# Kernel tuning notes

Measured on AMD Instinct MI355X. Metric: run time of the kernel, lower is better.

Reference implementation:

```python
import jax, jax.numpy as jnp
import numpy as np

B, N, D_IN, D_OUT = 8, 2048, 256, 128
ROW_ZERO = 85 - 10  # hardcoded in original: a[:, 0:85-10] = 0 (zeros rows, dim 1)
NEG_BIG = -9.0e15
EPS = 1e-12  # F.normalize eps


def setup_inputs() -> dict:
    key = jax.random.key(0)
    k1, k2, k3, k4 = jax.random.split(key, 4)
    h = jax.random.normal(k1, (B, N, D_IN), dtype=jnp.float32)
    adj = jax.random.randint(k2, (B, N, N), 0, 2, dtype=jnp.int32)
    adj_eye = jax.random.randint(k3, (B, N, N), 0, 2, dtype=jnp.int32)
    # xavier_uniform with gain=1.414 for W [in, out]
    limit = 1.414 * np.sqrt(6.0 / (D_IN + D_OUT))
    W = jax.random.uniform(k4, (D_IN, D_OUT), minval=-limit, maxval=limit, dtype=jnp.float32)
    return {"h": h, "adj": adj, "adj_eye": adj_eye, "W": W}


def reference(h, adj, adj_eye, W):
    # Wh: [B, N, D_OUT]
    Wh = jnp.matmul(h, W)
    # L2-normalize along feature dim (F.normalize semantics: x / max(||x||, eps))
    norm = jnp.maximum(jnp.linalg.norm(Wh, axis=-1, keepdims=True), EPS)
    Whn = Wh / norm
    # dense cosine-similarity scores: [B, N, N]
    score = jnp.einsum("bnd,bmd->bnm", Whn, Whn)
    # double-sort top-k emulation (faithful to original, incl. row-wise zeroing bug)
    a_sorted = jnp.sort(score, axis=-1)
    idx1 = jnp.argsort(score, axis=-1)
    a_sorted = a_sorted.at[:, 0:ROW_ZERO, :].set(0.0)
    idx2 = jnp.argsort(idx1, axis=-1)  # inverse permutation
    attscore = jnp.take_along_axis(a_sorted, idx2, axis=-1)
    # adjacency mask + softmax over neighbors
    e = jnp.where(adj_eye > 0, attscore, NEG_BIG)
    attention = jax.nn.softmax(e, axis=-1)
    # (dropout is identity in eval mode)
    h_prime = jnp.matmul(attention, Wh)
    return jax.nn.elu(h_prime)
```

## Files before the change

### kernel.cpp

```cpp
#include <hip/hip_runtime.h>
#include <stdint.h>

#define NN   2048
#define DD   128
#define DIN  256
#define ROWZ 75

typedef float f32x4 __attribute__((ext_vector_type(4)));
typedef short bf16x8 __attribute__((ext_vector_type(8)));
typedef unsigned int u32x2 __attribute__((ext_vector_type(2)));

__device__ __forceinline__ unsigned short f2bf(float x){
  union { float f; unsigned int u; } v; v.f = x;
  unsigned int u = v.u;
  u += 0x7fffu + ((u >> 16) & 1u);
  return (unsigned short)(u >> 16);
}
__device__ __forceinline__ float bf2f(unsigned short b){
  union { float f; unsigned int u; } v; v.u = ((unsigned int)b) << 16;
  return v.f;
}

__launch_bounds__(256, 2)
__global__ void wh_kernel(const float* __restrict__ h, const float* __restrict__ W,
                          unsigned short* __restrict__ whn, unsigned short* __restrict__ whT)
{
  __shared__ float hs[32][36];
  __shared__ float Ws[32][128];
  __shared__ float ssp[32][33];
  __shared__ float sinv[32];

  const int t  = threadIdx.x;
  const int bid = blockIdx.x;
  const int r0 = ((bid & 7) << 11) | ((bid >> 3) << 5);
  const int r4 = (t >> 5) * 4;
  const int d4 = (t & 31) * 4;

  float acc[4][4];
#pragma unroll
  for (int i = 0; i < 4; ++i)
#pragma unroll
    for (int j = 0; j < 4; ++j) acc[i][j] = 0.f;

  const int lrow = t >> 3;
  const int lkb  = (t & 7) * 4;
  const int wk   = t >> 3;
  const int wd   = (t & 7) * 16;

  f32x4 ph = *(const f32x4*)(h + (size_t)(r0 + lrow) * DIN + lkb);
  f32x4 pW[4];
  {
    const float* ws = W + (size_t)wk * DD + wd;
#pragma unroll
    for (int e = 0; e < 4; ++e) pW[e] = ((const f32x4*)ws)[e];
  }

  for (int kt = 0; kt < 8; ++kt){
    __syncthreads();
#pragma unroll
    for (int e = 0; e < 4; ++e) hs[lkb + e][lrow] = ph[e];
    {
      f32x4* dst = (f32x4*)&Ws[wk][wd];
#pragma unroll
      for (int e = 0; e < 4; ++e) dst[e] = pW[e];
    }
    __syncthreads();

    if (kt < 7){
      ph = *(const f32x4*)(h + (size_t)(r0 + lrow) * DIN + (kt+1)*32 + lkb);
      const float* ws = W + (size_t)((kt+1)*32 + wk) * DD + wd;
#pragma unroll
      for (int e = 0; e < 4; ++e) pW[e] = ((const f32x4*)ws)[e];
    }

#pragma unroll
    for (int k = 0; k < 32; ++k){
      f32x4 w4 = *(const f32x4*)&Ws[k][d4];
      f32x4 ha = *(const f32x4*)&hs[k][r4];
#pragma unroll
      for (int i = 0; i < 4; ++i)
#pragma unroll
        for (int j = 0; j < 4; ++j)
          acc[i][j] += ha[i] * w4[j];
    }
  }

#pragma unroll
  for (int i = 0; i < 4; ++i){
    float s = acc[i][0]*acc[i][0] + acc[i][1]*acc[i][1]
            + acc[i][2]*acc[i][2] + acc[i][3]*acc[i][3];
    ssp[r4 + i][t & 31] = s;
  }
  __syncthreads();
  if (t < 32){
    float ss = 0.f;
#pragma unroll
    for (int c = 0; c < 32; ++c) ss += ssp[t][c];
    sinv[t] = 1.0f / fmaxf(sqrtf(ss), 1e-12f);
  }
  __syncthreads();

  const int bb = r0 >> 11;
  const int n0 = (r0 & 2047) + r4;

#pragma unroll
  for (int i = 0; i < 4; ++i){
    const float inv = sinv[r4 + i];
    unsigned int lo = (unsigned int)f2bf(acc[i][0]*inv) | ((unsigned int)f2bf(acc[i][1]*inv) << 16);
    unsigned int hi = (unsigned int)f2bf(acc[i][2]*inv) | ((unsigned int)f2bf(acc[i][3]*inv) << 16);
    u32x2 pk = { lo, hi };
    *(u32x2*)(whn + (size_t)(r0 + r4 + i) * DD + d4) = pk;
  }
#pragma unroll
  for (int j = 0; j < 4; ++j){
    u32x2 pk;
#pragma unroll
    for (int e = 0; e < 2; ++e)
      pk[e] = (unsigned int)f2bf(acc[2*e][j]) | ((unsigned int)f2bf(acc[2*e + 1][j]) << 16);
    *(u32x2*)(whT + ((size_t)(bb * DD + d4 + j)) * NN + n0) = pk;
  }
}

__launch_bounds__(512, 2)
__global__ void attn_kernel(const unsigned short* __restrict__ whn,
                            const unsigned short* __restrict__ whT,
                            const int* __restrict__ adje,
                            float* __restrict__ out)
{
  __shared__ unsigned short Kt[2][128 * 128];
  __shared__ unsigned short Vt[2][128 * 128];
  __shared__ unsigned short Pbuf[8][32 * 40];
  __shared__ float linv_s[64];

  const int t    = threadIdx.x;
  const int w    = t >> 6;
  const int l    = t & 63;
  const int quad = l >> 4;
  const int l16  = l & 15;
  const int qh   = w >> 2;
  const int ms   = w & 3;
  const int b     = blockIdx.x & 7;
  const int qbase = (blockIdx.x >> 3) * 64;

  const unsigned short* whn_b = whn + (size_t)b * NN * DD;
  const unsigned short* whT_b = whT + (size_t)b * DD * NN;
  const int*            adj_b = adje + (size_t)b * NN * NN;

#define STAGE(M0, CC)                                                          \
  if (w < 4){                                                                  \
    _Pragma("unroll")                                                          \
    for (int ii = 0; ii < 8; ++ii){                                            \
      const int row = w*32 + ii*4 + (l >> 4);                                  \
      const unsigned short* src = whn_b + (size_t)((M0) + row) * DD            \
                                  + (l16 ^ (row & 7)) * 8;                     \
      __builtin_amdgcn_global_load_lds(                                        \
          (const __attribute__((address_space(1))) void*)src,                  \
          (__attribute__((address_space(3))) void*)&Kt[CC][(w*32 + ii*4)*128], \
          16, 0, 0);                                                           \
    }                                                                          \
  } else {                                                                     \
    _Pragma("unroll")                                                          \
    for (int ii = 0; ii < 8; ++ii){                                            \
      const int dv = (w-4)*32 + ii*4 + (l >> 4);                               \
      const unsigned short* src = whT_b + (size_t)dv * NN + (M0)               \
                                  + (l16 ^ (dv & 7)) * 8;                      \
      __builtin_amdgcn_global_load_lds(                                        \
          (const __attribute__((address_space(1))) void*)src,                  \
          (__attribute__((address_space(3))) void*)&Vt[CC][((w-4)*32+ii*4)*128],\
          16, 0, 0);                                                           \
    }                                                                          \
  }

  bf16x8 qf[2][4];
#pragma unroll
  for (int s = 0; s < 2; ++s)
#pragma unroll
    for (int kc = 0; kc < 4; ++kc)
      qf[s][kc] = *(const bf16x8*)(whn_b + (size_t)(qbase + qh*32 + s*16 + l16) * DD + kc*32 + quad*8);

  f32x4 oacc[2][8];
  float lacc[2][4];
#pragma unroll
  for (int s = 0; s < 2; ++s){
#pragma unroll
    for (int dt = 0; dt < 8; ++dt) oacc[s][dt] = (f32x4){0.f, 0.f, 0.f, 0.f};
#pragma unroll
    for (int r = 0; r < 4; ++r) lacc[s][r] = 0.f;
  }

  unsigned short* const Pw = &Pbuf[w][0];

  int av[2][2][4];
#pragma unroll
  for (int f = 0; f < 2; ++f)
#pragma unroll
    for (int s = 0; s < 2; ++s)
#pragma unroll
      for (int r = 0; r < 4; ++r)
        av[f][s][r] = adj_b[(size_t)(qbase + qh*32 + s*16 + quad*4 + r) * NN + ms*32 + f*16 + l16];
  STAGE(0, 0)
  __syncthreads();

  for (int it = 0; it < 16; ++it){
    const int m0  = it * 128;
    const int cur = it & 1;

    int avn[2][2][4];
    if (it < 15){
      const int mn = m0 + 128;
#pragma unroll
      for (int f = 0; f < 2; ++f)
#pragma unroll
        for (int s = 0; s < 2; ++s)
#pragma unroll
          for (int r = 0; r < 4; ++r)
            avn[f][s][r] = adj_b[(size_t)(qbase + qh*32 + s*16 + quad*4 + r) * NN + mn + ms*32 + f*16 + l16];
      STAGE(mn, cur ^ 1)
    }

    bf16x8 kf[2][4];
#pragma unroll
    for (int f = 0; f < 2; ++f)
#pragma unroll
      for (int kc = 0; kc < 4; ++kc){
        const int row = ms*32 + f*16 + l16;
        kf[f][kc] = *(const bf16x8*)&Kt[cur][row*128 + (((kc*4 + quad) ^ (l16 & 7)) * 8)];
      }
#pragma unroll
    for (int f = 0; f < 2; ++f){
#pragma unroll
      for (int s = 0; s < 2; ++s){
        f32x4 sc = (f32x4){0.f, 0.f, 0.f, 0.f};
#pragma unroll
        for (int kc = 0; kc < 4; ++kc)
          sc = __builtin_amdgcn_mfma_f32_16x16x32_bf16(qf[s][kc], kf[f][kc], sc, 0, 0, 0);
#pragma unroll
        for (int r = 0; r < 4; ++r){
          const int qrow = qbase + qh*32 + s*16 + quad*4 + r;
          float sv = (qrow < ROWZ) ? 0.f : sc[r];
          float p32 = (av[f][s][r] > 0) ? __expf(sv) : 0.f;
          unsigned short pb = f2bf(p32);
          lacc[s][r] += bf2f(pb);
          Pw[(s*16 + quad*4 + r) * 40 + f*16 + l16] = pb;
        }
      }
    }

    bf16x8 pfr0 = *(const bf16x8*)&Pw[(l16) * 40 + quad*8];
    bf16x8 pfr1 = *(const bf16x8*)&Pw[(16 + l16) * 40 + quad*8];
    __builtin_amdgcn_s_setprio(1);
#pragma unroll
    for (int dt = 0; dt < 8; ++dt){
      const int d = dt*16 + l16;
      bf16x8 vf = *(const bf16x8*)&Vt[cur][d*128 + (((ms*4 + quad) ^ (l16 & 7)) * 8)];
      oacc[0][dt] = __builtin_amdgcn_mfma_f32_16x16x32_bf16(pfr0, vf, oacc[0][dt], 0, 0, 0);
      oacc[1][dt] = __builtin_amdgcn_mfma_f32_16x16x32_bf16(pfr1, vf, oacc[1][dt], 0, 0, 0);
    }
    __builtin_amdgcn_s_setprio(0);

    __builtin_amdgcn_sched_barrier(0);
    asm volatile("s_waitcnt vmcnt(0)" ::: "memory");
    __builtin_amdgcn_sched_barrier(0);
    __builtin_amdgcn_s_barrier();
    __builtin_amdgcn_sched_barrier(0);

    if (it < 15){
#pragma unroll
      for (int f = 0; f < 2; ++f)
#pragma unroll
        for (int s = 0; s < 2; ++s)
#pragma unroll
          for (int r = 0; r < 4; ++r)
            av[f][s][r] = avn[f][s][r];
    }
  }

  {
    float* fl = (float*)&Pbuf[0][0];
#pragma unroll
    for (int s = 0; s < 2; ++s)
#pragma unroll
      for (int r = 0; r < 4; ++r)
        fl[(qh*32 + s*16 + quad*4 + r) * 64 + ms*16 + l16] = lacc[s][r];
  }
  __syncthreads();
  if (t < 64){
    const float* fl = (const float*)&Pbuf[0][0];
    float sum = 0.f;
#pragma unroll
    for (int c = 0; c < 64; ++c) sum += fl[t * 64 + c];
    linv_s[t] = 1.0f / sum;
  }

  float* const owf = (float*)&Kt[0][0];
  for (int s = 0; s < 2; ++s){
    __syncthreads();
#pragma unroll
    for (int dt = 0; dt < 8; ++dt)
#pragma unroll
      for (int r = 0; r < 4; ++r)
        owf[w*2048 + (quad*4 + r)*128 + dt*16 + l16] = oacc[s][dt][r];
    __syncthreads();
#pragma unroll
    for (int j = 0; j < 8; ++j){
      const int o     = j*512 + t;
      const int row32 = o >> 7;
      const int d     = o & 127;
      const int qh2   = row32 >> 4;
      const int r16   = row32 & 15;
      float v = owf[(qh2*4 + 0)*2048 + r16*128 + d]
              + owf[(qh2*4 + 1)*2048 + r16*128 + d]
              + owf[(qh2*4 + 2)*2048 + r16*128 + d]
              + owf[(qh2*4 + 3)*2048 + r16*128 + d];
      const int qrl = qh2*32 + s*16 + r16;
      v *= linv_s[qrl];
      v = (v > 0.f) ? v : expm1f(v);
      out[(size_t)(b*NN + qbase + qrl) * DD + d] = v;
    }
  }
#undef STAGE
}

extern "C" void kernel_launch(void* const* d_in, const int* in_sizes, int n_in,
                              void* d_out, int out_size, void* d_ws, size_t ws_size,
                              hipStream_t stream)
{
  const float* h       = (const float*)d_in[0];
  const int*   adj_eye = (const int*)d_in[2];
  const float* W       = (const float*)d_in[3];
  float*       out     = (float*)d_out;

  unsigned short* whn  = (unsigned short*)d_ws;
  unsigned short* whT  = whn + (size_t)16384 * 128;

  wh_kernel<<<512, 256, 0, stream>>>(h, W, whn, whT);
  attn_kernel<<<256, 512, 0, stream>>>(whn, whT, adj_eye, out);
}
```

Measured before the change: 285.8 us.

## Load K and V fragments directly from global, drop LDS double-buffering and barriers

Removes the double-buffered LDS staging of K and V tiles and the per-iteration vmcnt wait and block barrier. Each wave now loads its K and V MFMA fragments straight from global memory, relying on L2/L1 for reuse. Adjacency values are read as int2 pairs with a permuted column mapping, and the P row sum now accumulates the fp32 values instead of the bf16-rounded ones. This cuts LDS use and barrier stalls, but it increases redundant global/L2 traffic across waves and exposes load latency with no explicit prefetch.

Result: slower. 319.0 us (+11.6%).

```diff
diff --git a/kernel.cpp b/kernel.cpp
--- a/kernel.cpp
+++ b/kernel.cpp
@@ -8,6 +8,7 @@
 
 typedef float f32x4 __attribute__((ext_vector_type(4)));
 typedef short bf16x8 __attribute__((ext_vector_type(8)));
+typedef int   i32x2  __attribute__((ext_vector_type(2)));
 typedef unsigned int u32x2 __attribute__((ext_vector_type(2)));
 
 __device__ __forceinline__ unsigned short f2bf(float x){
@@ -15,10 +16,6 @@
   unsigned int u = v.u;
   u += 0x7fffu + ((u >> 16) & 1u);
   return (unsigned short)(u >> 16);
-}
-__device__ __forceinline__ float bf2f(unsigned short b){
-  union { float f; unsigned int u; } v; v.u = ((unsigned int)b) << 16;
-  return v.f;
 }
 
 __launch_bounds__(256, 2)
@@ -127,9 +124,7 @@
                             const int* __restrict__ adje,
                             float* __restrict__ out)
 {
-  __shared__ unsigned short Kt[2][128 * 128];
-  __shared__ unsigned short Vt[2][128 * 128];
-  __shared__ unsigned short Pbuf[8][32 * 40];
+  __shared__ float smem[16384];
   __shared__ float linv_s[64];
 
   const int t    = threadIdx.x;
@@ -146,30 +141,7 @@
   const unsigned short* whT_b = whT + (size_t)b * DD * NN;
   const int*            adj_b = adje + (size_t)b * NN * NN;
 
-#define STAGE(M0, CC)                                                          \
-  if (w < 4){                                                                  \
-    _Pragma("unroll")                                                          \
-    for (int ii = 0; ii < 8; ++ii){                                            \
-      const int row = w*32 + ii*4 + (l >> 4);                                  \
-      const unsigned short* src = whn_b + (size_t)((M0) + row) * DD            \
-                                  + (l16 ^ (row & 7)) * 8;                     \
-      __builtin_amdgcn_global_load_lds(                                        \
-          (const __attribute__((address_space(1))) void*)src,                  \
-          (__attribute__((address_space(3))) void*)&Kt[CC][(w*32 + ii*4)*128], \
-          16, 0, 0);                                                           \
-    }                                                                          \
-  } else {                                                                     \
-    _Pragma("unroll")                                                          \
-    for (int ii = 0; ii < 8; ++ii){                                            \
-      const int dv = (w-4)*32 + ii*4 + (l >> 4);                               \
-      const unsigned short* src = whT_b + (size_t)dv * NN + (M0)               \
-                                  + (l16 ^ (dv & 7)) * 8;                      \
-      __builtin_amdgcn_global_load_lds(                                        \
-          (const __attribute__((address_space(1))) void*)src,                  \
-          (__attribute__((address_space(3))) void*)&Vt[CC][((w-4)*32+ii*4)*128],\
-          16, 0, 0);                                                           \
-    }                                                                          \
-  }
+  unsigned short* const Pw = (unsigned short*)smem + w * (32 * 40);
 
   bf16x8 qf[2][4];
 #pragma unroll
@@ -188,95 +160,86 @@
     for (int r = 0; r < 4; ++r) lacc[s][r] = 0.f;
   }
 
-  unsigned short* const Pw = &Pbuf[w][0];
-
-  int av[2][2][4];
-#pragma unroll
-  for (int f = 0; f < 2; ++f)
-#pragma unroll
-    for (int s = 0; s < 2; ++s)
-#pragma unroll
-      for (int r = 0; r < 4; ++r)
-        av[f][s][r] = adj_b[(size_t)(qbase + qh*32 + s*16 + quad*4 + r) * NN + ms*32 + f*16 + l16];
-  STAGE(0, 0)
-  __syncthreads();
+  bool zr[2][4];
+#pragma unroll
+  for (int s = 0; s < 2; ++s)
+#pragma unroll
+    for (int r = 0; r < 4; ++r)
+      zr[s][r] = (qbase + qh*32 + s*16 + quad*4 + r) < ROWZ;
+
+  i32x2 av[2][4];
+#pragma unroll
+  for (int s = 0; s < 2; ++s)
+#pragma unroll
+    for (int r = 0; r < 4; ++r)
+      av[s][r] = *(const i32x2*)(adj_b + (size_t)(qbase + qh*32 + s*16 + quad*4 + r) * NN + ms*32 + 2*l16);
 
   for (int it = 0; it < 16; ++it){
-    const int m0  = it * 128;
-    const int cur = it & 1;
-
-    int avn[2][2][4];
+    const int m0 = it * 128;
+
+    bf16x8 kf[2][4];
+#pragma unroll
+    for (int f = 0; f < 2; ++f)
+#pragma unroll
+      for (int kc = 0; kc < 4; ++kc)
+        kf[f][kc] = *(const bf16x8*)(whn_b + (size_t)(m0 + ms*32 + 2*l16 + f) * DD + kc*32 + quad*8);
+
+    i32x2 avn[2][4];
     if (it < 15){
       const int mn = m0 + 128;
 #pragma unroll
-      for (int f = 0; f < 2; ++f)
-#pragma unroll
-        for (int s = 0; s < 2; ++s)
-#pragma unroll
-          for (int r = 0; r < 4; ++r)
-            avn[f][s][r] = adj_b[(size_t)(qbase + qh*32 + s*16 + quad*4 + r) * NN + mn + ms*32 + f*16 + l16];
-      STAGE(mn, cur ^ 1)
-    }
-
-    bf16x8 kf[2][4];
-#pragma unroll
-    for (int f = 0; f < 2; ++f)
+      for (int s = 0; s < 2; ++s)
+#pragma unroll
+        for (int r = 0; r < 4; ++r)
+          avn[s][r] = *(const i32x2*)(adj_b + (size_t)(qbase + qh*32 + s*16 + quad*4 + r) * NN + mn + ms*32 + 2*l16);
+    }
+
+#pragma unroll
+    for (int s = 0; s < 2; ++s){
+      f32x4 sc0 = (f32x4){0.f,0.f,0.f,0.f};
+      f32x4 sc1 = (f32x4){0.f,0.f,0.f,0.f};
 #pragma unroll
       for (int kc = 0; kc < 4; ++kc){
-        const int row = ms*32 + f*16 + l16;
-        kf[f][kc] = *(const bf16x8*)&Kt[cur][row*128 + (((kc*4 + quad) ^ (l16 & 7)) * 8)];
+        sc0 = __builtin_amdgcn_mfma_f32_16x16x32_bf16(qf[s][kc], kf[0][kc], sc0, 0, 0, 0);
+        sc1 = __builtin_amdgcn_mfma_f32_16x16x32_bf16(qf[s][kc], kf[1][kc], sc1, 0, 0, 0);
       }
 #pragma unroll
-    for (int f = 0; f < 2; ++f){
-#pragma unroll
-      for (int s = 0; s < 2; ++s){
-        f32x4 sc = (f32x4){0.f, 0.f, 0.f, 0.f};
-#pragma unroll
-        for (int kc = 0; kc < 4; ++kc)
-          sc = __builtin_amdgcn_mfma_f32_16x16x32_bf16(qf[s][kc], kf[f][kc], sc, 0, 0, 0);
-#pragma unroll
-        for (int r = 0; r < 4; ++r){
-          const int qrow = qbase + qh*32 + s*16 + quad*4 + r;
-          float sv = (qrow < ROWZ) ? 0.f : sc[r];
-          float p32 = (av[f][s][r] > 0) ? __expf(sv) : 0.f;
-          unsigned short pb = f2bf(p32);
-          lacc[s][r] += bf2f(pb);
-          Pw[(s*16 + quad*4 + r) * 40 + f*16 + l16] = pb;
-        }
+      for (int r = 0; r < 4; ++r){
+        float sv0 = zr[s][r] ? 0.f : sc0[r];
+        float sv1 = zr[s][r] ? 0.f : sc1[r];
+        float p0 = (av[s][r].x > 0) ? __expf(sv0) : 0.f;
+        float p1 = (av[s][r].y > 0) ? __expf(sv1) : 0.f;
+        lacc[s][r] += p0 + p1;
+        unsigned int pk = (unsigned int)f2bf(p0) | ((unsigned int)f2bf(p1) << 16);
+        *(unsigned int*)&Pw[(s*16 + quad*4 + r) * 40 + 2*l16] = pk;
       }
     }
 
     bf16x8 pfr0 = *(const bf16x8*)&Pw[(l16) * 40 + quad*8];
     bf16x8 pfr1 = *(const bf16x8*)&Pw[(16 + l16) * 40 + quad*8];
+    bf16x8 vf[8];
+#pragma unroll
+    for (int dt = 0; dt < 8; ++dt)
+      vf[dt] = *(const bf16x8*)(whT_b + (size_t)(dt*16 + l16) * NN + m0 + ms*32 + quad*8);
     __builtin_amdgcn_s_setprio(1);
 #pragma unroll
     for (int dt = 0; dt < 8; ++dt){
-      const int d = dt*16 + l16;
-      bf16x8 vf = *(const bf16x8*)&Vt[cur][d*128 + (((ms*4 + quad) ^ (l16 & 7)) * 8)];
-      oacc[0][dt] = __builtin_amdgcn_mfma_f32_16x16x32_bf16(pfr0, vf, oacc[0][dt], 0, 0, 0);
-      oacc[1][dt] = __builtin_amdgcn_mfma_f32_16x16x32_bf16(pfr1, vf, oacc[1][dt], 0, 0, 0);
+      oacc[0][dt] = __builtin_amdgcn_mfma_f32_16x16x32_bf16(pfr0, vf[dt], oacc[0][dt], 0, 0, 0);
+      oacc[1][dt] = __builtin_amdgcn_mfma_f32_16x16x32_bf16(pfr1, vf[dt], oacc[1][dt], 0, 0, 0);
     }
     __builtin_amdgcn_s_setprio(0);
 
-    __builtin_amdgcn_sched_barrier(0);
-    asm volatile("s_waitcnt vmcnt(0)" ::: "memory");
-    __builtin_amdgcn_sched_barrier(0);
-    __builtin_amdgcn_s_barrier();
-    __builtin_amdgcn_sched_barrier(0);
-
-    if (it < 15){
-#pragma unroll
-      for (int f = 0; f < 2; ++f)
-#pragma unroll
-        for (int s = 0; s < 2; ++s)
-#pragma unroll
-          for (int r = 0; r < 4; ++r)
-            av[f][s][r] = avn[f][s][r];
-    }
-  }
+#pragma unroll
+    for (int s = 0; s < 2; ++s)
+#pragma unroll
+      for (int r = 0; r < 4; ++r)
+        av[s][r] = avn[s][r];
+  }
+
+  __syncthreads();
 
   {
-    float* fl = (float*)&Pbuf[0][0];
+    float* fl = smem;
 #pragma unroll
     for (int s = 0; s < 2; ++s)
 #pragma unroll
@@ -285,14 +248,14 @@
   }
   __syncthreads();
   if (t < 64){
-    const float* fl = (const float*)&Pbuf[0][0];
+    const float* fl = smem;
     float sum = 0.f;
 #pragma unroll
     for (int c = 0; c < 64; ++c) sum += fl[t * 64 + c];
     linv_s[t] = 1.0f / sum;
   }
 
-  float* const owf = (float*)&Kt[0][0];
+  float* const owf = smem;
   for (int s = 0; s < 2; ++s){
     __syncthreads();
 #pragma unroll
@@ -318,7 +281,6 @@
       out[(size_t)(b*NN + qbase + qrl) * DD + d] = v;
     }
   }
-#undef STAGE
 }
 
 extern "C" void kernel_launch(void* const* d_in, const int* in_sizes, int n_in,
```

## Compute Wh projection with split-bf16 MFMA instead of scalar FP32 FMA

Applied to the files above, without the earlier changes.

The h·W projection kernel now splits each fp32 operand into bf16 hi and lo parts and accumulates three bf16 MFMA products, giving near-fp32 accuracy on the matrix cores instead of scalar FMAs. It computes both Wh and its transpose directly in MFMA layouts and reduces the row norms with shuffles. Blocks change to 64 rows and 512 threads. The projection is a small share of total time and the output stores are narrower and less coalesced, so the overall gain is bounded.

After: 282.7 us. No clear change (-1.1%).

```diff
diff --git a/kernel.cpp b/kernel.cpp
--- a/kernel.cpp
+++ b/kernel.cpp
@@ -21,104 +21,122 @@
   return v.f;
 }
 
-__launch_bounds__(256, 2)
+__launch_bounds__(512, 2)
 __global__ void wh_kernel(const float* __restrict__ h, const float* __restrict__ W,
                           unsigned short* __restrict__ whn, unsigned short* __restrict__ whT)
 {
-  __shared__ float hs[32][36];
-  __shared__ float Ws[32][128];
-  __shared__ float ssp[32][33];
-  __shared__ float sinv[32];
-
-  const int t  = threadIdx.x;
-  const int bid = blockIdx.x;
-  const int r0 = ((bid & 7) << 11) | ((bid >> 3) << 5);
-  const int r4 = (t >> 5) * 4;
-  const int d4 = (t & 31) * 4;
-
-  float acc[4][4];
-#pragma unroll
-  for (int i = 0; i < 4; ++i)
-#pragma unroll
-    for (int j = 0; j < 4; ++j) acc[i][j] = 0.f;
-
-  const int lrow = t >> 3;
-  const int lkb  = (t & 7) * 4;
-  const int wk   = t >> 3;
-  const int wd   = (t & 7) * 16;
-
-  f32x4 ph = *(const f32x4*)(h + (size_t)(r0 + lrow) * DIN + lkb);
-  f32x4 pW[4];
-  {
-    const float* ws = W + (size_t)wk * DD + wd;
-#pragma unroll
-    for (int e = 0; e < 4; ++e) pW[e] = ((const f32x4*)ws)[e];
-  }
+  __shared__ unsigned short WhiT[128][40];
+  __shared__ unsigned short WloT[128][40];
+  __shared__ float ssp[64][3];
+  __shared__ float sinv_s[64];
+
+  const int t    = threadIdx.x;
+  const int bid  = blockIdx.x;
+  const int r0   = ((bid & 7) << 11) | ((bid >> 3) << 6);
+  const int w    = t >> 6;
+  const int l    = t & 63;
+  const int quad = l >> 4;
+  const int l16  = l & 15;
+  const int wr   = (w & 3) * 16;
+  const int nc   = (w >> 2) * 64;
+  const int ch   = w >> 2;
+
+  const int sd = t & 127;
+  const int sk = (t >> 7) * 8;
+
+  f32x4 acc[4], occ[4];
+#pragma unroll
+  for (int ns = 0; ns < 4; ++ns){
+    acc[ns] = (f32x4){0.f,0.f,0.f,0.f};
+    occ[ns] = (f32x4){0.f,0.f,0.f,0.f};
+  }
+
+  float wv[8];
+#pragma unroll
+  for (int j = 0; j < 8; ++j) wv[j] = W[(size_t)(sk + j) * DD + sd];
+  const float* hrow = h + (size_t)(r0 + wr + l16) * DIN;
+  f32x4 hv0 = *(const f32x4*)(hrow + quad*8);
+  f32x4 hv1 = *(const f32x4*)(hrow + quad*8 + 4);
 
   for (int kt = 0; kt < 8; ++kt){
     __syncthreads();
-#pragma unroll
-    for (int e = 0; e < 4; ++e) hs[lkb + e][lrow] = ph[e];
     {
-      f32x4* dst = (f32x4*)&Ws[wk][wd];
-#pragma unroll
-      for (int e = 0; e < 4; ++e) dst[e] = pW[e];
+      bf16x8 whi8, wlo8;
+#pragma unroll
+      for (int j = 0; j < 8; ++j){
+        float x = wv[j];
+        unsigned short hb = f2bf(x);
+        whi8[j] = (short)hb;
+        wlo8[j] = (short)f2bf(x - bf2f(hb));
+      }
+      *(bf16x8*)&WhiT[sd][sk] = whi8;
+      *(bf16x8*)&WloT[sd][sk] = wlo8;
+    }
+    bf16x8 ahi, alo;
+#pragma unroll
+    for (int e = 0; e < 4; ++e){
+      unsigned short hb0 = f2bf(hv0[e]), hb1 = f2bf(hv1[e]);
+      ahi[e]   = (short)hb0;  alo[e]   = (short)f2bf(hv0[e] - bf2f(hb0));
+      ahi[4+e] = (short)hb1;  alo[4+e] = (short)f2bf(hv1[e] - bf2f(hb1));
     }
     __syncthreads();
 
     if (kt < 7){
-      ph = *(const f32x4*)(h + (size_t)(r0 + lrow) * DIN + (kt+1)*32 + lkb);
-      const float* ws = W + (size_t)((kt+1)*32 + wk) * DD + wd;
-#pragma unroll
-      for (int e = 0; e < 4; ++e) pW[e] = ((const f32x4*)ws)[e];
-    }
-
-#pragma unroll
-    for (int k = 0; k < 32; ++k){
-      f32x4 w4 = *(const f32x4*)&Ws[k][d4];
-      f32x4 ha = *(const f32x4*)&hs[k][r4];
-#pragma unroll
-      for (int i = 0; i < 4; ++i)
-#pragma unroll
-        for (int j = 0; j < 4; ++j)
-          acc[i][j] += ha[i] * w4[j];
-    }
-  }
-
-#pragma unroll
-  for (int i = 0; i < 4; ++i){
-    float s = acc[i][0]*acc[i][0] + acc[i][1]*acc[i][1]
-            + acc[i][2]*acc[i][2] + acc[i][3]*acc[i][3];
-    ssp[r4 + i][t & 31] = s;
+      const int k0n = (kt + 1) * 32;
+#pragma unroll
+      for (int j = 0; j < 8; ++j) wv[j] = W[(size_t)(k0n + sk + j) * DD + sd];
+      hv0 = *(const f32x4*)(hrow + k0n + quad*8);
+      hv1 = *(const f32x4*)(hrow + k0n + quad*8 + 4);
+    }
+
+#pragma unroll
+    for (int ns = 0; ns < 4; ++ns){
+      bf16x8 bhi = *(const bf16x8*)&WhiT[nc + ns*16 + l16][quad*8];
+      bf16x8 blo = *(const bf16x8*)&WloT[nc + ns*16 + l16][quad*8];
+      acc[ns] = __builtin_amdgcn_mfma_f32_16x16x32_bf16(ahi, bhi, acc[ns], 0, 0, 0);
+      acc[ns] = __builtin_amdgcn_mfma_f32_16x16x32_bf16(alo, bhi, acc[ns], 0, 0, 0);
+      acc[ns] = __builtin_amdgcn_mfma_f32_16x16x32_bf16(ahi, blo, acc[ns], 0, 0, 0);
+      occ[ns] = __builtin_amdgcn_mfma_f32_16x16x32_bf16(bhi, ahi, occ[ns], 0, 0, 0);
+      occ[ns] = __builtin_amdgcn_mfma_f32_16x16x32_bf16(bhi, alo, occ[ns], 0, 0, 0);
+      occ[ns] = __builtin_amdgcn_mfma_f32_16x16x32_bf16(blo, ahi, occ[ns], 0, 0, 0);
+    }
+  }
+
+#pragma unroll
+  for (int r = 0; r < 4; ++r){
+    float val = 0.f;
+#pragma unroll
+    for (int ns = 0; ns < 4; ++ns) val += acc[ns][r] * acc[ns][r];
+    val += __shfl_xor(val, 1);
+    val += __shfl_xor(val, 2);
+    val += __shfl_xor(val, 4);
+    val += __shfl_xor(val, 8);
+    if (l16 == 0) ssp[wr + quad*4 + r][ch] = val;
   }
   __syncthreads();
-  if (t < 32){
-    float ss = 0.f;
-#pragma unroll
-    for (int c = 0; c < 32; ++c) ss += ssp[t][c];
-    sinv[t] = 1.0f / fmaxf(sqrtf(ss), 1e-12f);
+  if (t < 64){
+    float ss = ssp[t][0] + ssp[t][1];
+    sinv_s[t] = 1.0f / fmaxf(sqrtf(ss), 1e-12f);
   }
   __syncthreads();
 
   const int bb = r0 >> 11;
-  const int n0 = (r0 & 2047) + r4;
-
-#pragma unroll
-  for (int i = 0; i < 4; ++i){
-    const float inv = sinv[r4 + i];
-    unsigned int lo = (unsigned int)f2bf(acc[i][0]*inv) | ((unsigned int)f2bf(acc[i][1]*inv) << 16);
-    unsigned int hi = (unsigned int)f2bf(acc[i][2]*inv) | ((unsigned int)f2bf(acc[i][3]*inv) << 16);
-    u32x2 pk = { lo, hi };
-    *(u32x2*)(whn + (size_t)(r0 + r4 + i) * DD + d4) = pk;
-  }
-#pragma unroll
-  for (int j = 0; j < 4; ++j){
-    u32x2 pk;
-#pragma unroll
-    for (int e = 0; e < 2; ++e)
-      pk[e] = (unsigned int)f2bf(acc[2*e][j]) | ((unsigned int)f2bf(acc[2*e + 1][j]) << 16);
-    *(u32x2*)(whT + ((size_t)(bb * DD + d4 + j)) * NN + n0) = pk;
-  }
+  const int n0 = (r0 & 2047) + wr;
+
+#pragma unroll
+  for (int ns = 0; ns < 4; ++ns)
+#pragma unroll
+    for (int r = 0; r < 4; ++r){
+      const int row = wr + quad*4 + r;
+      whn[(size_t)(r0 + row) * DD + nc + ns*16 + l16] = f2bf(acc[ns][r] * sinv_s[row]);
+    }
+#pragma unroll
+  for (int ns = 0; ns < 4; ++ns)
+#pragma unroll
+    for (int r = 0; r < 4; ++r){
+      const int d = nc + ns*16 + quad*4 + r;
+      whT[((size_t)(bb * DD + d)) * NN + n0 + l16] = f2bf(occ[ns][r]);
+    }
 }
 
 __launch_bounds__(512, 2)
@@ -333,6 +351,6 @@
   unsigned short* whn  = (unsigned short*)d_ws;
   unsigned short* whT  = whn + (size_t)16384 * 128;
 
-  wh_kernel<<<512, 256, 0, stream>>>(h, W, whn, whT);
+  wh_kernel<<<256, 512, 0, stream>>>(h, W, whn, whT);
   attn_kernel<<<256, 512, 0, stream>>>(whn, whT, adj_eye, out);
 }
```
